# Performance work log

Hardware: AMD Instinct MI355X
Metric: run time of the kernel (lower is better)

The kernel has to match this reference:

```python
import jax, jax.numpy as jnp
import numpy as np

N_NODES = 50000
N_EDGES = 600000
N_GRAPHS = 500


def gcn_conv(x, src, dst, W, b, n_nodes):
    # PyG GCNConv: add self-loops, symmetric normalization D^-1/2 (A+I) D^-1/2, then XW + b
    h = x @ W  # [N, F_out]
    loop = jnp.arange(n_nodes)
    s = jnp.concatenate([src, loop])
    d = jnp.concatenate([dst, loop])
    deg = jax.ops.segment_sum(jnp.ones_like(d, dtype=h.dtype), d, num_segments=n_nodes)
    dinv = jnp.where(deg > 0, jax.lax.rsqrt(jnp.maximum(deg, 1.0)), 0.0)
    norm = dinv[s] * dinv[d]  # [E+N]
    msg = h[s] * norm[:, None]  # gather + scale
    out = jax.ops.segment_sum(msg, d, num_segments=n_nodes)  # scatter-add
    return out + b


def setup_inputs() -> dict:
    key = jax.random.key(0)
    ks = jax.random.split(key, 12)
    F_in, H, Hf, D_out = 128, 128, 64, 1
    x = jax.random.normal(ks[0], (N_NODES, F_in), dtype=jnp.float32)
    edge_index = jax.random.randint(ks[1], (2, N_EDGES), 0, N_NODES, dtype=jnp.int64)
    batch = jnp.sort(jax.random.randint(ks[2], (N_NODES,), 0, N_GRAPHS, dtype=jnp.int64))
    def glorot(k, shape):
        lim = np.sqrt(6.0 / (shape[0] + shape[1]))
        return jax.random.uniform(k, shape, jnp.float32, -lim, lim)
    return {
        "x": x, "edge_index": edge_index, "batch": batch,
        "W1": glorot(ks[3], (F_in, H)), "b1": jnp.zeros((H,), jnp.float32),
        "W2": glorot(ks[4], (H, H)), "b2": jnp.zeros((H,), jnp.float32),
        "W3": glorot(ks[5], (H, H)), "b3": jnp.zeros((H,), jnp.float32),
        "Wf1": glorot(ks[6], (H, Hf)), "bf1": jnp.zeros((Hf,), jnp.float32),
        "Wf2": glorot(ks[7], (Hf, D_out)), "bf2": jnp.zeros((D_out,), jnp.float32),
    }


def reference(x, edge_index, batch, W1, b1, W2, b2, W3, b3, Wf1, bf1, Wf2, bf2):
    src, dst = edge_index[0], edge_index[1]
    n = x.shape[0]
    h = jax.nn.relu(gcn_conv(x, src, dst, W1, b1, n))
    h = jax.nn.relu(gcn_conv(h, src, dst, W2, b2, n))
    h = jax.nn.relu(gcn_conv(h, src, dst, W3, b3, n))
    # global_mean_pool: segment mean over graphs
    sums = jax.ops.segment_sum(h, batch, num_segments=N_GRAPHS)
    cnts = jax.ops.segment_sum(jnp.ones((n,), h.dtype), batch, num_segments=N_GRAPHS)
    hg = sums / jnp.maximum(cnts, 1.0)[:, None]  # [G, 128]
    h = jax.nn.relu(hg @ Wf1 + bf1)
    return h @ Wf2 + bf2
```

## Files before the change

kernel.cpp:

```cpp
#include <hip/hip_runtime.h>

#define N_NODES 50000
#define N_EDGES 600000
#define N_GRAPHS 500
#define F 128

typedef short bf16x8 __attribute__((ext_vector_type(8)));
typedef float f32x4 __attribute__((ext_vector_type(4)));
union U4H8 { uint4 u; bf16x8 h; };

__device__ inline unsigned pk_bf16(float a, float b) {
    unsigned ua = __float_as_uint(a), ub = __float_as_uint(b);
    ua = (ua + 0x7fffu + ((ua >> 16) & 1u)) >> 16;
    ub = (ub + 0x7fffu + ((ub >> 16) & 1u)) >> 16;
    return ua | (ub << 16);
}
__device__ inline float bf16_rnd(float x) {
    unsigned u = __float_as_uint(x);
    u = (u + 0x7fffu + ((u >> 16) & 1u)) & 0xffff0000u;
    return __uint_as_float(u);
}
#define BF_LO(u) __uint_as_float((u) << 16)
#define BF_HI(u) __uint_as_float((u) & 0xffff0000u)

#define G_CVT  3125
#define G_HIST 2344
#define G_PREPW 24

__global__ __launch_bounds__(256) void k_prep(const float* __restrict__ x, unsigned short* __restrict__ xb,
                                              const int* __restrict__ dst, int* __restrict__ cnt,
                                              const float* __restrict__ W1, const float* __restrict__ W2,
                                              const float* __restrict__ W3,
                                              uint4* __restrict__ Whi, uint4* __restrict__ Wlo) {
    int b = blockIdx.x, tid = threadIdx.x;
    if (b < G_CVT) {
        int idx = b * 256 + tid;
        if (idx < N_NODES * F / 8) {
            const float4* xr = (const float4*)(x + (size_t)idx * 8);
            float4 a = xr[0], c = xr[1];
            uint4 o;
            o.x = pk_bf16(a.x, a.y); o.y = pk_bf16(a.z, a.w);
            o.z = pk_bf16(c.x, c.y); o.w = pk_bf16(c.z, c.w);
            ((uint4*)xb)[idx] = o;
        }
    } else if (b < G_CVT + G_HIST) {
        int e = (b - G_CVT) * 256 + tid;
        if (e < N_EDGES) atomicAdd(&cnt[dst[e]], 1);
    } else {
        int idx = (b - G_CVT - G_HIST) * 256 + tid;
        int layer = idx >> 11;
        const float* W = (layer == 0) ? W1 : (layer == 1) ? W2 : W3;
        int t = idx & 2047;
        int lane = t & 63, sc = t >> 6;
        int s = sc >> 3, c = sc & 7;
        int q = lane >> 4, m = lane & 15;
        int k0 = 32 * s + 8 * q, n0 = 16 * c + m;
        float w[8], h[8];
        #pragma unroll
        for (int j = 0; j < 8; ++j) {
            w[j] = W[(k0 + j) * F + n0];
            h[j] = bf16_rnd(w[j]);
        }
        uint4 uh, ul;
        uh.x = pk_bf16(h[0], h[1]); uh.y = pk_bf16(h[2], h[3]);
        uh.z = pk_bf16(h[4], h[5]); uh.w = pk_bf16(h[6], h[7]);
        ul.x = pk_bf16(w[0] - h[0], w[1] - h[1]); ul.y = pk_bf16(w[2] - h[2], w[3] - h[3]);
        ul.z = pk_bf16(w[4] - h[4], w[5] - h[5]); ul.w = pk_bf16(w[6] - h[6], w[7] - h[7]);
        Whi[idx] = uh;
        Wlo[idx] = ul;
    }
}

__global__ __launch_bounds__(256) void k_scan1(const int* __restrict__ cnt, int* __restrict__ row_ptr,
                                               int* __restrict__ blksums, float* __restrict__ dinv, int n) {
    __shared__ int s[256];
    int i = blockIdx.x * 256 + threadIdx.x;
    int v = (i < n) ? cnt[i] : 0;
    if (i < n) dinv[i] = rsqrtf((float)(v + 1));
    s[threadIdx.x] = v;
    __syncthreads();
    for (int off = 1; off < 256; off <<= 1) {
        int t = (threadIdx.x >= off) ? s[threadIdx.x - off] : 0;
        __syncthreads();
        s[threadIdx.x] += t;
        __syncthreads();
    }
    if (i < n) row_ptr[i] = s[threadIdx.x] - v;
    if (threadIdx.x == 255) blksums[blockIdx.x] = s[255];
}

__global__ __launch_bounds__(256) void k_scan2(int* __restrict__ blksums, int nb) {
    __shared__ int s[256];
    int v = (threadIdx.x < nb) ? blksums[threadIdx.x] : 0;
    s[threadIdx.x] = v;
    __syncthreads();
    for (int off = 1; off < 256; off <<= 1) {
        int t = (threadIdx.x >= off) ? s[threadIdx.x - off] : 0;
        __syncthreads();
        s[threadIdx.x] += t;
        __syncthreads();
    }
    if (threadIdx.x < nb) blksums[threadIdx.x] = s[threadIdx.x] - v;
}

__global__ __launch_bounds__(256) void k_scan3(int* __restrict__ row_ptr, const int* __restrict__ blksums,
                                               int n, int ne) {
    int i = blockIdx.x * 256 + threadIdx.x;
    if (i < n) row_ptr[i] += blksums[blockIdx.x];
    if (i == 0) row_ptr[n] = ne;
}

__global__ __launch_bounds__(256) void k_fill(const int* __restrict__ src, const int* __restrict__ dst,
                                              const int* __restrict__ row_ptr, int* __restrict__ cnt,
                                              const float* __restrict__ dinv,
                                              int2* __restrict__ esw, int ne) {
    int e = blockIdx.x * 256 + threadIdx.x;
    if (e < ne) {
        int d = dst[e];
        int s = src[e];
        int pos = row_ptr[d] + atomicSub(&cnt[d], 1) - 1;
        esw[pos] = make_int2(s, __float_as_int(dinv[s]));
    }
}

#define TN 32
#define GP 132
__global__ __launch_bounds__(256) void k_fused(const int* __restrict__ row_ptr,
                                               const int2* __restrict__ esw,
                                               const float* __restrict__ dinv,
                                               const unsigned short* __restrict__ Hin,
                                               const uint4* __restrict__ Whi,
                                               const uint4* __restrict__ Wlo,
                                               const float* __restrict__ bias,
                                               unsigned short* __restrict__ Hout, int n) {
    __shared__ float G[TN * GP];
    int tid = threadIdx.x;
    int d0 = blockIdx.x * TN;
    int grp = tid >> 4, sub = tid & 15;

    #pragma unroll
    for (int i = 0; i < 2; ++i) {
        int nl = 2 * grp + i;
        int node = d0 + nl;
        float4 accL = make_float4(0.f, 0.f, 0.f, 0.f);
        float4 accH = make_float4(0.f, 0.f, 0.f, 0.f);
        if (node < n) {
            int beg = row_ptr[node], end = row_ptr[node + 1];
            float dd = dinv[node];
            int e = beg + sub;
            int2 rec;
            if (e < end)       rec = esw[e];
            else if (e == end) rec = make_int2(node, __float_as_int(dd));
            else               rec = make_int2(0, 0);
            for (int c = beg; c <= end; c += 16) {
                #pragma unroll
                for (int hb = 0; hb < 2; ++hb) {
                    int j0 = hb * 8;
                    int sjs[8];
                    #pragma unroll
                    for (int j = 0; j < 8; ++j) sjs[j] = __shfl(rec.x, j0 + j, 16);
                    uint4 rows[8];
                    #pragma unroll
                    for (int j = 0; j < 8; ++j)
                        rows[j] = ((const uint4*)(Hin + (size_t)sjs[j] * F))[sub];
                    float wjs[8];
                    #pragma unroll
                    for (int j = 0; j < 8; ++j)
                        wjs[j] = __uint_as_float((unsigned)__shfl(rec.y, j0 + j, 16)) * dd;
                    #pragma unroll
                    for (int j = 0; j < 8; ++j) {
                        float wj = wjs[j];
                        accL.x = fmaf(BF_LO(rows[j].x), wj, accL.x);
                        accL.y = fmaf(BF_HI(rows[j].x), wj, accL.y);
                        accL.z = fmaf(BF_LO(rows[j].y), wj, accL.z);
                        accL.w = fmaf(BF_HI(rows[j].y), wj, accL.w);
                        accH.x = fmaf(BF_LO(rows[j].z), wj, accH.x);
                        accH.y = fmaf(BF_HI(rows[j].z), wj, accH.y);
                        accH.z = fmaf(BF_LO(rows[j].w), wj, accH.z);
                        accH.w = fmaf(BF_HI(rows[j].w), wj, accH.w);
                    }
                }
                if (c + 16 <= end) {
                    int e2 = c + 16 + sub;
                    if (e2 < end)       rec = esw[e2];
                    else if (e2 == end) rec = make_int2(node, __float_as_int(dd));
                    else                rec = make_int2(0, 0);
                }
            }
        }
        float* gr = &G[nl * GP + 8 * sub];
        ((float4*)gr)[0] = accL;
        ((float4*)gr)[1] = accH;
    }
    __syncthreads();

    int wave = tid >> 6, lane = tid & 63;
    int q = lane >> 4, m = lane & 15;
    int rt = wave & 1;
    int ch = (wave >> 1) * 4;
    int row0 = 16 * rt;
    f32x4 acc[4];
    #pragma unroll
    for (int c = 0; c < 4; ++c) acc[c] = (f32x4){0.f, 0.f, 0.f, 0.f};
    #pragma unroll
    for (int s = 0; s < 4; ++s) {
        const float* gr = &G[(row0 + m) * GP + 32 * s + 8 * q];
        float4 f0 = ((const float4*)gr)[0];
        float4 f1 = ((const float4*)gr)[1];
        float h0 = bf16_rnd(f0.x), h1 = bf16_rnd(f0.y), h2 = bf16_rnd(f0.z), h3 = bf16_rnd(f0.w);
        float h4 = bf16_rnd(f1.x), h5 = bf16_rnd(f1.y), h6 = bf16_rnd(f1.z), h7 = bf16_rnd(f1.w);
        U4H8 ahi, alo;
        ahi.u.x = (__float_as_uint(h0) >> 16) | (__float_as_uint(h1) & 0xffff0000u);
        ahi.u.y = (__float_as_uint(h2) >> 16) | (__float_as_uint(h3) & 0xffff0000u);
        ahi.u.z = (__float_as_uint(h4) >> 16) | (__float_as_uint(h5) & 0xffff0000u);
        ahi.u.w = (__float_as_uint(h6) >> 16) | (__float_as_uint(h7) & 0xffff0000u);
        alo.u.x = pk_bf16(f0.x - h0, f0.y - h1);
        alo.u.y = pk_bf16(f0.z - h2, f0.w - h3);
        alo.u.z = pk_bf16(f1.x - h4, f1.y - h5);
        alo.u.w = pk_bf16(f1.z - h6, f1.w - h7);
        #pragma unroll
        for (int cc = 0; cc < 4; ++cc) {
            int c = ch + cc;
            U4H8 bh, bl;
            bh.u = Whi[(s * 8 + c) * 64 + lane];
            bl.u = Wlo[(s * 8 + c) * 64 + lane];
            acc[cc] = __builtin_amdgcn_mfma_f32_16x16x32_bf16(ahi.h, bh.h, acc[cc], 0, 0, 0);
            acc[cc] = __builtin_amdgcn_mfma_f32_16x16x32_bf16(alo.h, bh.h, acc[cc], 0, 0, 0);
            acc[cc] = __builtin_amdgcn_mfma_f32_16x16x32_bf16(ahi.h, bl.h, acc[cc], 0, 0, 0);
        }
    }
    __syncthreads();

    #pragma unroll
    for (int cc = 0; cc < 4; ++cc) {
        int c = ch + cc;
        float bb = bias[16 * c + m];
        #pragma unroll
        for (int r = 0; r < 4; ++r)
            G[(row0 + 4 * q + r) * GP + 16 * c + m] = fmaxf(acc[cc][r] + bb, 0.f);
    }
    __syncthreads();
    #pragma unroll
    for (int j = 0; j < 2; ++j) {
        int lin = tid + 256 * j;
        int row = lin >> 4, c8 = lin & 15;
        int node = d0 + row;
        if (node < n) {
            const float* gr = &G[row * GP + c8 * 8];
            uint4 o;
            o.x = pk_bf16(gr[0], gr[1]);
            o.y = pk_bf16(gr[2], gr[3]);
            o.z = pk_bf16(gr[4], gr[5]);
            o.w = pk_bf16(gr[6], gr[7]);
            ((uint4*)(Hout + (size_t)node * F))[c8] = o;
        }
    }
}

__global__ __launch_bounds__(256) void k_pool_fc(const unsigned short* __restrict__ Hb,
                                                 const int* __restrict__ batch,
                                                 const float* __restrict__ Wf1,
                                                 const float* __restrict__ bf1,
                                                 const float* __restrict__ Wf2,
                                                 const float* __restrict__ bf2,
                                                 float* __restrict__ out) {
    int g = blockIdx.x;
    int tid = threadIdx.x;
    int lo = 0, hi = N_NODES;
    while (lo < hi) { int mid = (lo + hi) >> 1; if (batch[mid] < g) lo = mid + 1; else hi = mid; }
    int start = lo;
    hi = N_NODES;
    while (lo < hi) { int mid = (lo + hi) >> 1; if (batch[mid] <= g) lo = mid + 1; else hi = mid; }
    int end = lo;

    __shared__ float hs[4][F];
    __shared__ float hg[F];
    int wv = tid >> 6, lane = tid & 63;
    int half = lane >> 5, sub = lane & 31;
    float4 a = make_float4(0.f, 0.f, 0.f, 0.f);
    for (int i = start + wv * 2 + half; i < end; i += 8) {
        uint2 v = ((const uint2*)(Hb + (size_t)i * F))[sub];
        a.x += BF_LO(v.x); a.y += BF_HI(v.x);
        a.z += BF_LO(v.y); a.w += BF_HI(v.y);
    }
    a.x += __shfl_xor(a.x, 32, 64);
    a.y += __shfl_xor(a.y, 32, 64);
    a.z += __shfl_xor(a.z, 32, 64);
    a.w += __shfl_xor(a.w, 32, 64);
    if (half == 0) ((float4*)hs[wv])[sub] = a;
    __syncthreads();
    if (tid < F) {
        float inv = 1.0f / (float)((end - start) > 0 ? (end - start) : 1);
        hg[tid] = (hs[0][tid] + hs[1][tid] + hs[2][tid] + hs[3][tid]) * inv;
    }
    __syncthreads();
    if (tid < 64) {
        float acc = bf1[tid];
        #pragma unroll 4
        for (int f = 0; f < F; ++f) acc = fmaf(hg[f], Wf1[f * 64 + tid], acc);
        float v = fmaxf(acc, 0.f) * Wf2[tid];
        #pragma unroll
        for (int off = 32; off > 0; off >>= 1) v += __shfl_down(v, off, 64);
        if (tid == 0) out[g] = v + bf2[0];
    }
}

extern "C" void kernel_launch(void* const* d_in, const int* in_sizes, int n_in,
                              void* d_out, int out_size, void* d_ws, size_t ws_size,
                              hipStream_t stream) {
    const float* x    = (const float*)d_in[0];
    const int* eidx   = (const int*)d_in[1];
    const int* batch  = (const int*)d_in[2];
    const float* W1   = (const float*)d_in[3];
    const float* b1   = (const float*)d_in[4];
    const float* W2   = (const float*)d_in[5];
    const float* b2   = (const float*)d_in[6];
    const float* W3   = (const float*)d_in[7];
    const float* b3   = (const float*)d_in[8];
    const float* Wf1  = (const float*)d_in[9];
    const float* bf1  = (const float*)d_in[10];
    const float* Wf2  = (const float*)d_in[11];
    const float* bf2  = (const float*)d_in[12];
    float* out = (float*)d_out;

    const int* src = eidx;
    const int* dst = eidx + N_EDGES;

    char* p = (char*)d_ws;
    unsigned short* Xb  = (unsigned short*)p;  p += (size_t)N_NODES * F * 2;
    unsigned short* H1  = (unsigned short*)p;  p += (size_t)N_NODES * F * 2;
    unsigned short* H2  = (unsigned short*)p;  p += (size_t)N_NODES * F * 2;
    unsigned short* H3  = (unsigned short*)p;  p += (size_t)N_NODES * F * 2;
    int2* esw   = (int2*)p;    p += (size_t)N_EDGES * sizeof(int2);
    uint4* Whi  = (uint4*)p;   p += (size_t)3 * 2048 * sizeof(uint4);
    uint4* Wlo  = (uint4*)p;   p += (size_t)3 * 2048 * sizeof(uint4);
    float* dinv = (float*)p;   p += (size_t)N_NODES * sizeof(float);
    int* cnt     = (int*)p;    p += (size_t)N_NODES * sizeof(int);
    int* row_ptr = (int*)p;    p += (size_t)(N_NODES + 1) * sizeof(int);
    int* blksums = (int*)p;    p += 256 * sizeof(int);

    dim3 b256(256);
    int gNodes = (N_NODES + 255) / 256;
    int gEdges = (N_EDGES + 255) / 256;
    int gFused = (N_NODES + TN - 1) / TN;

    hipMemsetAsync(cnt, 0, (size_t)N_NODES * sizeof(int), stream);
    k_prep<<<G_CVT + G_HIST + G_PREPW, b256, 0, stream>>>(x, Xb, dst, cnt, W1, W2, W3, Whi, Wlo);

    k_scan1<<<gNodes, b256, 0, stream>>>(cnt, row_ptr, blksums, dinv, N_NODES);
    k_scan2<<<1, b256, 0, stream>>>(blksums, gNodes);
    k_scan3<<<gNodes, b256, 0, stream>>>(row_ptr, blksums, N_NODES, N_EDGES);
    k_fill<<<gEdges, b256, 0, stream>>>(src, dst, row_ptr, cnt, dinv, esw, N_EDGES);

    k_fused<<<gFused, b256, 0, stream>>>(row_ptr, esw, dinv, Xb, Whi,        Wlo,        b1, H1, N_NODES);
    k_fused<<<gFused, b256, 0, stream>>>(row_ptr, esw, dinv, H1, Whi + 2048, Wlo + 2048, b2, H2, N_NODES);
    k_fused<<<gFused, b256, 0, stream>>>(row_ptr, esw, dinv, H2, Whi + 4096, Wlo + 4096, b3, H3, N_NODES);

    k_pool_fc<<<N_GRAPHS, b256, 0, stream>>>(H3, batch, Wf1, bf1, Wf2, bf2, out);
}
```

Measured before the change: 286.0 us.

## Stage block edge lists in LDS, peel self-loop, merge scan kernels

```diff
diff --git a/kernel.cpp b/kernel.cpp
--- a/kernel.cpp
+++ b/kernel.cpp
@@ -89,24 +89,19 @@
     if (threadIdx.x == 255) blksums[blockIdx.x] = s[255];
 }
 
-__global__ __launch_bounds__(256) void k_scan2(int* __restrict__ blksums, int nb) {
+__global__ __launch_bounds__(256) void k_scan23(int* __restrict__ row_ptr, const int* __restrict__ blksums,
+                                                int n, int ne) {
     __shared__ int s[256];
-    int v = (threadIdx.x < nb) ? blksums[threadIdx.x] : 0;
-    s[threadIdx.x] = v;
-    __syncthreads();
-    for (int off = 1; off < 256; off <<= 1) {
-        int t = (threadIdx.x >= off) ? s[threadIdx.x - off] : 0;
+    int tid = threadIdx.x;
+    s[tid] = (tid < (int)blockIdx.x) ? blksums[tid] : 0;
+    __syncthreads();
+    for (int off = 128; off > 0; off >>= 1) {
+        if (tid < off) s[tid] += s[tid + off];
         __syncthreads();
-        s[threadIdx.x] += t;
-        __syncthreads();
-    }
-    if (threadIdx.x < nb) blksums[threadIdx.x] = s[threadIdx.x] - v;
-}
-
-__global__ __launch_bounds__(256) void k_scan3(int* __restrict__ row_ptr, const int* __restrict__ blksums,
-                                               int n, int ne) {
-    int i = blockIdx.x * 256 + threadIdx.x;
-    if (i < n) row_ptr[i] += blksums[blockIdx.x];
+    }
+    int base = s[0];
+    int i = blockIdx.x * 256 + tid;
+    if (i < n) row_ptr[i] += base;
     if (i == 0) row_ptr[n] = ne;
 }
 
@@ -125,6 +120,7 @@
 
 #define TN 32
 #define GP 132
+#define MAXE_L 1024
 __global__ __launch_bounds__(256) void k_fused(const int* __restrict__ row_ptr,
                                                const int2* __restrict__ esw,
                                                const float* __restrict__ dinv,
@@ -134,8 +130,27 @@
                                                const float* __restrict__ bias,
                                                unsigned short* __restrict__ Hout, int n) {
     __shared__ float G[TN * GP];
+    __shared__ uint2 eL[MAXE_L];
+    __shared__ int rp[TN + 1];
+    __shared__ float ddl[TN];
     int tid = threadIdx.x;
     int d0 = blockIdx.x * TN;
+
+    int dTN = d0 + TN; if (dTN > n) dTN = n;
+    int e0 = row_ptr[d0];
+    int e1 = row_ptr[dTN];
+    if (tid <= TN) {
+        int d = d0 + tid; if (d > n) d = n;
+        rp[tid] = row_ptr[d];
+    }
+    if (tid < TN) {
+        int d = d0 + tid;
+        ddl[tid] = (d < n) ? dinv[d] : 0.f;
+    }
+    int nE = e1 - e0; if (nE > MAXE_L) nE = MAXE_L;
+    for (int i = tid; i < nE; i += 256) eL[i] = ((const uint2*)esw)[e0 + i];
+    __syncthreads();
+
     int grp = tid >> 4, sub = tid & 15;
 
     #pragma unroll
@@ -145,46 +160,45 @@
         float4 accL = make_float4(0.f, 0.f, 0.f, 0.f);
         float4 accH = make_float4(0.f, 0.f, 0.f, 0.f);
         if (node < n) {
-            int beg = row_ptr[node], end = row_ptr[node + 1];
-            float dd = dinv[node];
-            int e = beg + sub;
-            int2 rec;
-            if (e < end)       rec = esw[e];
-            else if (e == end) rec = make_int2(node, __float_as_int(dd));
-            else               rec = make_int2(0, 0);
-            for (int c = beg; c <= end; c += 16) {
+            int beg = rp[nl], end = rp[nl + 1];
+            float dd = ddl[nl];
+            uint4 srow = ((const uint4*)(Hin + (size_t)node * F))[sub];
+            float ws = dd * dd;
+            accL.x = BF_LO(srow.x) * ws;
+            accL.y = BF_HI(srow.x) * ws;
+            accL.z = BF_LO(srow.y) * ws;
+            accL.w = BF_HI(srow.y) * ws;
+            accH.x = BF_LO(srow.z) * ws;
+            accH.y = BF_HI(srow.z) * ws;
+            accH.z = BF_LO(srow.w) * ws;
+            accH.w = BF_HI(srow.w) * ws;
+            for (int c = beg; c < end; c += 8) {
+                uint2 recs[8];
                 #pragma unroll
-                for (int hb = 0; hb < 2; ++hb) {
-                    int j0 = hb * 8;
-                    int sjs[8];
-                    #pragma unroll
-                    for (int j = 0; j < 8; ++j) sjs[j] = __shfl(rec.x, j0 + j, 16);
-                    uint4 rows[8];
-                    #pragma unroll
-                    for (int j = 0; j < 8; ++j)
-                        rows[j] = ((const uint4*)(Hin + (size_t)sjs[j] * F))[sub];
-                    float wjs[8];
-                    #pragma unroll
-                    for (int j = 0; j < 8; ++j)
-                        wjs[j] = __uint_as_float((unsigned)__shfl(rec.y, j0 + j, 16)) * dd;
-                    #pragma unroll
-                    for (int j = 0; j < 8; ++j) {
-                        float wj = wjs[j];
-                        accL.x = fmaf(BF_LO(rows[j].x), wj, accL.x);
-                        accL.y = fmaf(BF_HI(rows[j].x), wj, accL.y);
-                        accL.z = fmaf(BF_LO(rows[j].y), wj, accL.z);
-                        accL.w = fmaf(BF_HI(rows[j].y), wj, accL.w);
-                        accH.x = fmaf(BF_LO(rows[j].z), wj, accH.x);
-                        accH.y = fmaf(BF_HI(rows[j].z), wj, accH.y);
-                        accH.z = fmaf(BF_LO(rows[j].w), wj, accH.z);
-                        accH.w = fmaf(BF_HI(rows[j].w), wj, accH.w);
+                for (int j = 0; j < 8; ++j) {
+                    int e = c + j;
+                    uint2 r = make_uint2((unsigned)node, 0u);
+                    if (e < end) {
+                        int off = e - e0;
+                        r = (off < MAXE_L) ? eL[off] : ((const uint2*)esw)[e];
                     }
+                    recs[j] = r;
                 }
-                if (c + 16 <= end) {
-                    int e2 = c + 16 + sub;
-                    if (e2 < end)       rec = esw[e2];
-                    else if (e2 == end) rec = make_int2(node, __float_as_int(dd));
-                    else                rec = make_int2(0, 0);
+                uint4 rows[8];
+                #pragma unroll
+                for (int j = 0; j < 8; ++j)
+                    rows[j] = ((const uint4*)(Hin + (size_t)recs[j].x * F))[sub];
+                #pragma unroll
+                for (int j = 0; j < 8; ++j) {
+                    float wj = __uint_as_float(recs[j].y) * dd;
+                    accL.x = fmaf(BF_LO(rows[j].x), wj, accL.x);
+                    accL.y = fmaf(BF_HI(rows[j].x), wj, accL.y);
+                    accL.z = fmaf(BF_LO(rows[j].y), wj, accL.z);
+                    accL.w = fmaf(BF_HI(rows[j].y), wj, accL.w);
+                    accH.x = fmaf(BF_LO(rows[j].z), wj, accH.x);
+                    accH.y = fmaf(BF_HI(rows[j].z), wj, accH.y);
+                    accH.z = fmaf(BF_LO(rows[j].w), wj, accH.z);
+                    accH.w = fmaf(BF_HI(rows[j].w), wj, accH.w);
                 }
             }
         }
@@ -348,8 +362,7 @@
     k_prep<<<G_CVT + G_HIST + G_PREPW, b256, 0, stream>>>(x, Xb, dst, cnt, W1, W2, W3, Whi, Wlo);
 
     k_scan1<<<gNodes, b256, 0, stream>>>(cnt, row_ptr, blksums, dinv, N_NODES);
-    k_scan2<<<1, b256, 0, stream>>>(blksums, gNodes);
-    k_scan3<<<gNodes, b256, 0, stream>>>(row_ptr, blksums, N_NODES, N_EDGES);
+    k_scan23<<<gNodes, b256, 0, stream>>>(row_ptr, blksums, N_NODES, N_EDGES);
     k_fill<<<gEdges, b256, 0, stream>>>(src, dst, row_ptr, cnt, dinv, esw, N_EDGES);
 
     k_fused<<<gFused, b256, 0, stream>>>(row_ptr, esw, dinv, Xb, Whi,        Wlo,        b1, H1, N_NODES);
```

Result: faster. 273.5 us (-4.4%).
